# Kernel optimization log

Hardware: AMD Instinct MI355X
Metric: run time of the kernel (lower is better)

Reference implementation:

```python
import jax, jax.numpy as jnp
import numpy as np

B, T = 64, 2048
HID, FAST, SLOW, VOCAB = 256, 64, 256, 64
WRITE_THRESH = 0.4
NEG = -1000000000.0


def setup_inputs() -> dict:
    key = jax.random.key(0)
    ks = jax.random.split(key, 10)
    s = 0.05  # small init so gate sigmoids are not saturated
    return {
        "seq": jax.random.randint(ks[0], (B, T), 0, VOCAB),
        "emb": jax.random.normal(ks[1], (VOCAB, HID), jnp.float32),        # encoder embedding table
        "Wg": jax.random.normal(ks[2], (HID, 1), jnp.float32) * s,         # write_gate
        "bg": jnp.zeros((1,), jnp.float32),
        "Wd": jax.random.normal(ks[3], (HID, 1), jnp.float32) * s,         # demotion_net
        "bd": jnp.zeros((1,), jnp.float32),
        "Wq": jax.random.normal(ks[4], (HID, HID), jnp.float32) * s,       # read_head.q_proj
        "bq": jnp.zeros((HID,), jnp.float32),
        "Wo": jax.random.normal(ks[5], (HID, VOCAB), jnp.float32) * s,     # read_head.out
        "bo": jnp.zeros((VOCAB,), jnp.float32),
    }


def _process_sequence(h, Wg, bg, Wd, bd):
    # h: (B, T, H). Sequential LRU tiered-memory scatter, vectorized over batch.
    Bb, Tt, H = h.shape

    def step(state, tok_h):
        fm, sm, fa, sa, fu, su = state
        ws = jax.nn.sigmoid(tok_h @ Wg + bg)[:, 0]          # (B,) write score
        act = ws >= WRITE_THRESH                            # skip rows with score < 0.4
        fa = fa + fu.astype(jnp.int32)                      # age occupied slots
        sa = sa + su.astype(jnp.int32)
        free = ~fu
        has_free = jnp.any(free, axis=1)                    # (B,)
        free_idx = jnp.argmax(free, axis=1)                 # first free fast slot
        dem = ((fm @ Wd)[..., 0] + bd[0])                   # (B, FAST) demotion scores
        dem_slot = jnp.argmin(dem, axis=1)
        fslot = jnp.where(has_free, free_idx, dem_slot)     # fast slot to write
        foh = jax.nn.one_hot(fslot, FAST, dtype=bool)
        wf = act[:, None] & foh                              # (B, FAST) fast-write mask
        # value demoted to slow (only used when fast was full)
        demoted = jnp.take_along_axis(fm, fslot[:, None, None], axis=1)[:, 0, :]
        slow_act = act & ~has_free
        sfree = ~su
        s_has_free = jnp.any(sfree, axis=1)
        ss = jnp.where(s_has_free, jnp.argmax(sfree, axis=1), jnp.argmax(sa, axis=1))
        soh = jax.nn.one_hot(ss, SLOW, dtype=bool)
        wsm = slow_act[:, None] & soh                        # (B, SLOW) slow-write mask
        sm = jnp.where(wsm[..., None], demoted[:, None, :], sm)
        sa = jnp.where(wsm, 0, sa)
        su = su | wsm
        tok = jax.lax.stop_gradient(tok_h)                   # original writes tok_h.detach()
        fm = jnp.where(wf[..., None], tok[:, None, :], fm)
        fa = jnp.where(wf, 0, fa)
        fu = fu | wf
        return (fm, sm, fa, sa, fu, su), None

    init = (
        jnp.zeros((Bb, FAST, H), h.dtype),
        jnp.zeros((Bb, SLOW, H), h.dtype),
        jnp.zeros((Bb, FAST), jnp.int32),
        jnp.zeros((Bb, SLOW), jnp.int32),
        jnp.zeros((Bb, FAST), bool),
        jnp.zeros((Bb, SLOW), bool),
    )
    hs = jnp.swapaxes(h[:, : Tt - 3], 0, 1)                  # loop runs for T-3 tokens
    (fm, sm, fa, sa, fu, su), _ = jax.lax.scan(step, init, hs)
    memory = jnp.concatenate([fm, sm], axis=1)               # (B, F+S, H)
    mask = jnp.concatenate([fu, su], axis=1).astype(h.dtype)
    slow_mask = su.astype(h.dtype)
    return memory, mask, slow_mask


def reference(seq, emb, Wg, bg, Wd, bd, Wq, bq, Wo, bo):
    h = emb[seq]                                             # encoder: (B, T, H)
    memory, mask, slow_mask = _process_sequence(h, Wg, bg, Wd, bd)
    # ReadHead
    q = h[:, -1, :] @ Wq + bq                                # (B, H)
    scores = jnp.einsum("bnh,bh->bn", memory, q)
    scores = jnp.where(mask == 0, NEG, scores)
    attn = jax.nn.softmax(scores, axis=-1)
    ctx = jnp.einsum("bn,bnh->bh", attn, memory)
    logits = ctx @ Wo + bo                                   # (B, VOCAB)
    return logits, slow_mask
```

## Files before the change

kernel.cpp:

```cpp
#include <hip/hip_runtime.h>
#include <math.h>

#define BB 64
#define TT 2048
#define HIDD 256
#define FASTN 64
#define SLOWN 256
#define VOC 64
#define TLOOP (TT - 3)
#define NEGC -1000000000.0f
#define EPAD 257
#define NEGBIG (-(1 << 20))
#define BYTEAT(U, J) ((int)(((U) >> (8 * (J))) & 0xFFu))

__global__ __launch_bounds__(256) void k_tab(
    const float* __restrict__ emb,
    const float* __restrict__ Wg, const float* __restrict__ bg,
    const float* __restrict__ Wd, const float* __restrict__ bd,
    const float* __restrict__ Wq, const float* __restrict__ bq,
    float* __restrict__ qTok, int* __restrict__ prG, int* __restrict__ invG) {
  const int tid = threadIdx.x;
  __shared__ float eS[HIDD];
  __shared__ float part[4][64];
  __shared__ float demS[64];

  if (blockIdx.x < 256) {
    const int u = blockIdx.x >> 2, jt = blockIdx.x & 3;
    eS[tid] = emb[u * HIDD + tid];
    __syncthreads();
    const int j = tid & 63, kp = tid >> 6;
    const float* w = &Wq[(kp * 64) * HIDD + jt * 64 + j];
    const float* e = &eS[kp * 64];
    float acc = 0.f;
#pragma unroll 8
    for (int kk = 0; kk < 64; ++kk) acc += e[kk] * w[kk * HIDD];
    part[kp][j] = acc;
    __syncthreads();
    if (tid < 64)
      qTok[u * HIDD + jt * 64 + tid] =
          part[0][tid] + part[1][tid] + part[2][tid] + part[3][tid] + bq[jt * 64 + tid];
  } else {
    const int v = tid & 63, kp = tid >> 6;
    const float* e = &emb[v * HIDD + kp * 64];
    const float* wg = &Wg[kp * 64];
    const float* wd = &Wd[kp * 64];
    float g = 0.f, d = 0.f;
#pragma unroll 8
    for (int k = 0; k < 64; ++k) { float ev = e[k]; g += ev * wg[k]; d += ev * wd[k]; }
    part[kp][v] = g;
    __syncthreads();
    __shared__ float dpart[4][64];
    dpart[kp][v] = d;
    __syncthreads();
    int myact = 0;
    if (tid < 64) {
      float gg = part[0][tid] + part[1][tid] + part[2][tid] + part[3][tid] + bg[0];
      float dd = dpart[0][tid] + dpart[1][tid] + dpart[2][tid] + dpart[3][tid] + bd[0];
      myact = (1.f / (1.f + expf(-gg)) >= 0.4f) ? 1 : 0;
      demS[tid] = dd;
    }
    __syncthreads();
    if (tid < 64) {
      float dv = demS[tid];
      int r = 0;
      for (int u2 = 0; u2 < 64; ++u2) {
        float du = demS[u2];
        r += (du < dv || (du == dv && u2 < tid)) ? 1 : 0;
      }
      prG[tid] = myact ? r : 0xFF;
      invG[r] = tid;
    }
  }
}

__global__ __launch_bounds__(512) void k_main(
    const int* __restrict__ seq, const float* __restrict__ emb,
    const float* __restrict__ qTok, const int* __restrict__ prG,
    const int* __restrict__ invG,
    const float* __restrict__ Wo, const float* __restrict__ bo,
    float* __restrict__ out) {
  const int b = blockIdx.x;
  const int tid = threadIdx.x;
  const int lane = tid & 63;
  const int wv = tid >> 6;

  __shared__ float embS[VOC * EPAD];
  __shared__ float WoS[HIDD * VOC];
  __shared__ __align__(16) unsigned char zsB[2080];
  __shared__ float qLastS[HIDD], ctxS[HIDD];
  __shared__ float pp[4][64];
  __shared__ float wS[64];
  __shared__ int prS[64], invS[64], cntTok[64];
  __shared__ int CS[8];
  __shared__ int PsS[8][64], QsS[8][64], aEndS[8][64], eSS[8][64];

  const int4 sq = ((const int4*)(seq + b * TT))[tid];
  const int lastv = seq[b * TT + TT - 1];
  if (tid < 64) { prS[tid] = prG[tid]; invS[tid] = invG[tid]; }
  if (tid < 256) qLastS[tid] = qTok[lastv * HIDD + tid];
  const float4* emb4 = (const float4*)emb;
  for (int i = tid; i < VOC * 64; i += 512) {
    float4 e = emb4[i];
    float* d = &embS[(i >> 6) * EPAD + ((i & 63) << 2)];
    d[0] = e.x; d[1] = e.y; d[2] = e.z; d[3] = e.w;
  }
  {
    const float4* Wo4 = (const float4*)Wo;
    float4* WoS4 = (float4*)WoS;
    for (int i = tid; i < HIDD * VOC / 4; i += 512) WoS4[i] = Wo4[i];
  }
  __syncthreads();

  const int t0 = tid * 4;
  int tk[4] = {sq.x, sq.y, sq.z, sq.w};
  int by[4]; int c = 0;
#pragma unroll
  for (int j = 0; j < 4; ++j) {
    int r = prS[tk[j]];
    by[j] = (t0 + j < TLOOP) ? r : 0xFF;
    c += (by[j] != 0xFF) ? 1 : 0;
  }
  int incl = c;
  for (int s = 1; s < 64; s <<= 1) {
    int t = __shfl_up(incl, s);
    if (lane >= s) incl += t;
  }
  if (lane == 63) CS[wv] = incl;
  __syncthreads();

  int Ow = 0, A = 0;
#pragma unroll
  for (int w2 = 0; w2 < 8; ++w2) {
    int cw = CS[w2];
    Ow += (w2 < wv) ? cw : 0;
    A += cw;
  }
  {
    int pos = Ow + incl - c;
#pragma unroll
    for (int j = 0; j < 4; ++j)
      if (by[j] != 0xFF) zsB[pos++] = (unsigned char)by[j];
  }
  __syncthreads();

  const int fsplit = A < 64 ? A : 64;
  const int nL = A - fsplit;
  const int win = nL < 256 ? nL : 256;
  const int wstart = A - win;
  const int L = (((A + 7) >> 3) + 15) & ~15;
  const int baseW = wv * L;
  const int endW = min(baseW + L, A);

  int P = 0, Q = NEGBIG;
  for (int g = baseW; g < endW; g += 16) {
    uint4 t4 = *(const uint4*)(zsB + g);
    unsigned dsw[4] = {t4.x, t4.y, t4.z, t4.w};
    const int gHi = min(g + 16, endW);
    if (gHi == g + 16 && gHi <= fsplit) {
#pragma unroll
      for (int d = 0; d < 4; ++d)
#pragma unroll
        for (int j = 0; j < 4; ++j) {
          int x = (BYTEAT(dsw[d], j) <= lane) ? 1 : 0;
          P += x; Q += x;
        }
    } else if (gHi == g + 16 && g >= fsplit) {
#pragma unroll
      for (int d = 0; d < 4; ++d)
#pragma unroll
        for (int j = 0; j < 4; ++j) {
          int x = (BYTEAT(dsw[d], j) <= lane) ? 1 : 0;
          P += x - 1;
          Q = max(Q + x - 1, x);
        }
    } else {
#pragma unroll
      for (int d = 0; d < 4; ++d)
#pragma unroll
        for (int j = 0; j < 4; ++j) {
          int i = g + d * 4 + j;
          int x = (BYTEAT(dsw[d], j) <= lane) ? 1 : 0;
          bool vld = i < endW;
          bool fil = i < fsplit;
          int p = fil ? x : x - 1;
          int q = fil ? NEGBIG : x;
          int Pn = P + p;
          int Qn = max(Q + p, q);
          P = vld ? Pn : P;
          Q = vld ? Qn : Q;
        }
    }
  }
  PsS[wv][lane] = P;
  QsS[wv][lane] = Q;
  __syncthreads();

  int a = 0;
  for (int w2 = 0; w2 < wv; ++w2)
    a = max(a + PsS[w2][lane], QsS[w2][lane]);

  int e = 0;
  for (int g = baseW; g < endW; g += 16) {
    uint4 t4 = *(const uint4*)(zsB + g);
    unsigned dsw[4] = {t4.x, t4.y, t4.z, t4.w};
    const int gHi = min(g + 16, endW);
    const bool full = (gHi == g + 16);
    if (full && gHi <= fsplit) {
#pragma unroll
      for (int d = 0; d < 4; ++d)
#pragma unroll
        for (int j = 0; j < 4; ++j)
          a += (BYTEAT(dsw[d], j) <= lane) ? 1 : 0;
    } else if (full && g >= fsplit && gHi <= wstart) {
#pragma unroll
      for (int d = 0; d < 4; ++d)
#pragma unroll
        for (int j = 0; j < 4; ++j) {
          int xm1 = (BYTEAT(dsw[d], j) <= lane) ? 0 : -1;
          a = max(a, 1) + xm1;
        }
    } else if (full && g >= wstart) {
#pragma unroll
      for (int d = 0; d < 4; ++d)
#pragma unroll
        for (int j = 0; j < 4; ++j) {
          int xm1 = (BYTEAT(dsw[d], j) <= lane) ? 0 : -1;
          e += (a > 0) ? 1 : 0;
          a = max(a, 1) + xm1;
        }
    } else {
#pragma unroll
      for (int d = 0; d < 4; ++d)
#pragma unroll
        for (int j = 0; j < 4; ++j) {
          int i = g + d * 4 + j;
          int x = (BYTEAT(dsw[d], j) <= lane) ? 1 : 0;
          bool vld = i < endW;
          bool fil = i < fsplit;
          bool wg = vld && (i >= wstart);
          e += (wg && a > 0) ? 1 : 0;
          int af = a + x;
          int al = max(a, 1) + (x - 1);
          int an = fil ? af : al;
          a = vld ? an : a;
        }
    }
  }
  aEndS[wv][lane] = a;
  eSS[wv][lane] = e;
  __syncthreads();

  if (tid < 64) {
    int af = aEndS[7][lane];
    int et = 0;
#pragma unroll
    for (int w2 = 0; w2 < 8; ++w2) et += eSS[w2][lane];
    int ap = __shfl_up(af, 1); if (lane == 0) ap = 0;
    int ep = __shfl_up(et, 1); if (lane == 0) ep = 0;
    cntTok[invS[lane]] = (af - ap) + (et - ep);
  }
  __syncthreads();

  if (tid < 256) {
    int v = tid & 63, part = tid >> 6;
    const float* er = &embS[v * EPAD + part * 64];
    const float* qr = &qLastS[part * 64];
    float s = 0.f;
#pragma unroll 8
    for (int k = 0; k < 64; ++k) s += er[k] * qr[k];
    pp[part][v] = s;
  }
  __syncthreads();
  if (tid < 64) {
    float sc = pp[0][tid] + pp[1][tid] + pp[2][tid] + pp[3][tid];
    int cc = cntTok[tid];
    float m = (cc > 0) ? sc : NEGC;
    for (int off = 32; off; off >>= 1) m = fmaxf(m, __shfl_xor(m, off));
    float w = (cc > 0) ? (float)cc * expf(sc - m) : 0.f;
    float z = w;
    for (int off = 32; off; off >>= 1) z += __shfl_xor(z, off);
    z += (float)(FASTN + SLOWN - (fsplit + win)) * expf(NEGC - m);
    wS[tid] = w / z;
  }
  __syncthreads();

  if (tid < 256) {
    float cacc = 0.f;
#pragma unroll 8
    for (int u = 0; u < 64; ++u) cacc += wS[u] * embS[u * EPAD + tid];
    ctxS[tid] = cacc;
  }
  __syncthreads();

  if (tid < 256) {
    int o = tid & 63, part = tid >> 6;
    const float* cr = &ctxS[part * 64];
    const float* wr = &WoS[part * 64 * VOC + o];
    float s = 0.f;
#pragma unroll 8
    for (int k = 0; k < 64; ++k) s += cr[k] * wr[k * VOC];
    pp[part][o] = s;
  }
  __syncthreads();
  if (tid < 64)
    out[b * VOC + tid] = pp[0][tid] + pp[1][tid] + pp[2][tid] + pp[3][tid] + bo[tid];
  if (tid < 256)
    out[BB * VOC + b * SLOWN + tid] = (tid < win) ? 1.0f : 0.0f;
}

extern "C" void kernel_launch(void* const* d_in, const int* in_sizes, int n_in,
                              void* d_out, int out_size, void* d_ws, size_t ws_size,
                              hipStream_t stream) {
  const int*   seq = (const int*)d_in[0];
  const float* emb = (const float*)d_in[1];
  const float* Wg  = (const float*)d_in[2];
  const float* bg  = (const float*)d_in[3];
  const float* Wd  = (const float*)d_in[4];
  const float* bd  = (const float*)d_in[5];
  const float* Wq  = (const float*)d_in[6];
  const float* bq  = (const float*)d_in[7];
  const float* Wo  = (const float*)d_in[8];
  const float* bo  = (const float*)d_in[9];
  float* out = (float*)d_out;

  char* ws = (char*)d_ws;
  float* qTok = (float*)ws;
  int*   prG  = (int*)(ws + 16384 * 4);
  int*   invG = (int*)(ws + 16448 * 4);

  k_tab<<<dim3(257), dim3(256), 0, stream>>>(emb, Wg, bg, Wd, bd, Wq, bq,
                                             qTok, prG, invG);
  k_main<<<dim3(64), dim3(512), 0, stream>>>(seq, emb, qTok, prG, invG,
                                             Wo, bo, out);
}
```

Measured before the change: 94.90 us.

## Fuse table precompute kernel into main kernel, computing per-block in shared memory

Removes the separate k_tab launch. Each block of the main kernel now computes the gate/demotion scores and rank tables from shared-memory embeddings, and only the query projection for its last token. This drops one kernel launch and the global workspace round trip, and avoids projecting all 64 vocab rows through Wq. The cost is redundant gate/rank computation in every block and a serial Wq read per block.

```diff
diff --git a/kernel.cpp b/kernel.cpp
--- a/kernel.cpp
+++ b/kernel.cpp
@@ -13,70 +13,11 @@
 #define NEGBIG (-(1 << 20))
 #define BYTEAT(U, J) ((int)(((U) >> (8 * (J))) & 0xFFu))
 
-__global__ __launch_bounds__(256) void k_tab(
-    const float* __restrict__ emb,
+__global__ __launch_bounds__(512) void k_one(
+    const int* __restrict__ seq, const float* __restrict__ emb,
     const float* __restrict__ Wg, const float* __restrict__ bg,
     const float* __restrict__ Wd, const float* __restrict__ bd,
     const float* __restrict__ Wq, const float* __restrict__ bq,
-    float* __restrict__ qTok, int* __restrict__ prG, int* __restrict__ invG) {
-  const int tid = threadIdx.x;
-  __shared__ float eS[HIDD];
-  __shared__ float part[4][64];
-  __shared__ float demS[64];
-
-  if (blockIdx.x < 256) {
-    const int u = blockIdx.x >> 2, jt = blockIdx.x & 3;
-    eS[tid] = emb[u * HIDD + tid];
-    __syncthreads();
-    const int j = tid & 63, kp = tid >> 6;
-    const float* w = &Wq[(kp * 64) * HIDD + jt * 64 + j];
-    const float* e = &eS[kp * 64];
-    float acc = 0.f;
-#pragma unroll 8
-    for (int kk = 0; kk < 64; ++kk) acc += e[kk] * w[kk * HIDD];
-    part[kp][j] = acc;
-    __syncthreads();
-    if (tid < 64)
-      qTok[u * HIDD + jt * 64 + tid] =
-          part[0][tid] + part[1][tid] + part[2][tid] + part[3][tid] + bq[jt * 64 + tid];
-  } else {
-    const int v = tid & 63, kp = tid >> 6;
-    const float* e = &emb[v * HIDD + kp * 64];
-    const float* wg = &Wg[kp * 64];
-    const float* wd = &Wd[kp * 64];
-    float g = 0.f, d = 0.f;
-#pragma unroll 8
-    for (int k = 0; k < 64; ++k) { float ev = e[k]; g += ev * wg[k]; d += ev * wd[k]; }
-    part[kp][v] = g;
-    __syncthreads();
-    __shared__ float dpart[4][64];
-    dpart[kp][v] = d;
-    __syncthreads();
-    int myact = 0;
-    if (tid < 64) {
-      float gg = part[0][tid] + part[1][tid] + part[2][tid] + part[3][tid] + bg[0];
-      float dd = dpart[0][tid] + dpart[1][tid] + dpart[2][tid] + dpart[3][tid] + bd[0];
-      myact = (1.f / (1.f + expf(-gg)) >= 0.4f) ? 1 : 0;
-      demS[tid] = dd;
-    }
-    __syncthreads();
-    if (tid < 64) {
-      float dv = demS[tid];
-      int r = 0;
-      for (int u2 = 0; u2 < 64; ++u2) {
-        float du = demS[u2];
-        r += (du < dv || (du == dv && u2 < tid)) ? 1 : 0;
-      }
-      prG[tid] = myact ? r : 0xFF;
-      invG[r] = tid;
-    }
-  }
-}
-
-__global__ __launch_bounds__(512) void k_main(
-    const int* __restrict__ seq, const float* __restrict__ emb,
-    const float* __restrict__ qTok, const int* __restrict__ prG,
-    const int* __restrict__ invG,
     const float* __restrict__ Wo, const float* __restrict__ bo,
     float* __restrict__ out) {
   const int b = blockIdx.x;
@@ -89,15 +30,15 @@
   __shared__ __align__(16) unsigned char zsB[2080];
   __shared__ float qLastS[HIDD], ctxS[HIDD];
   __shared__ float pp[4][64];
-  __shared__ float wS[64];
+  __shared__ float gp8[8][64], dp8[8][64];
+  __shared__ float qp2[2][HIDD];
+  __shared__ float demS[64], wS[64];
   __shared__ int prS[64], invS[64], cntTok[64];
   __shared__ int CS[8];
   __shared__ int PsS[8][64], QsS[8][64], aEndS[8][64], eSS[8][64];
 
   const int4 sq = ((const int4*)(seq + b * TT))[tid];
   const int lastv = seq[b * TT + TT - 1];
-  if (tid < 64) { prS[tid] = prG[tid]; invS[tid] = invG[tid]; }
-  if (tid < 256) qLastS[tid] = qTok[lastv * HIDD + tid];
   const float4* emb4 = (const float4*)emb;
   for (int i = tid; i < VOC * 64; i += 512) {
     float4 e = emb4[i];
@@ -108,6 +49,38 @@
     const float4* Wo4 = (const float4*)Wo;
     float4* WoS4 = (float4*)WoS;
     for (int i = tid; i < HIDD * VOC / 4; i += 512) WoS4[i] = Wo4[i];
+  }
+  __syncthreads();
+
+  {
+    const int v = tid & 63, kp = tid >> 6;
+    const float* er = &embS[v * EPAD + kp * 32];
+    const float* wg = &Wg[kp * 32];
+    const float* wd = &Wd[kp * 32];
+    float g = 0.f, d = 0.f;
+#pragma unroll 8
+    for (int k = 0; k < 32; ++k) { float e = er[k]; g += e * wg[k]; d += e * wd[k]; }
+    gp8[kp][v] = g; dp8[kp][v] = d;
+  }
+  __syncthreads();
+  if (tid < 64) {
+    float g = bg[0], d = bd[0];
+#pragma unroll
+    for (int p = 0; p < 8; ++p) { g += gp8[p][tid]; d += dp8[p][tid]; }
+    int act = (1.f / (1.f + expf(-g)) >= 0.4f) ? 1 : 0;
+    demS[tid] = d;
+    prS[tid] = act;
+  }
+  __syncthreads();
+  if (tid < 64) {
+    float dv = demS[tid];
+    int r = 0;
+    for (int u2 = 0; u2 < 64; ++u2) {
+      float du = demS[u2];
+      r += (du < dv || (du == dv && u2 < tid)) ? 1 : 0;
+    }
+    invS[r] = tid;
+    prS[tid] = prS[tid] ? r : 0xFF;
   }
   __syncthreads();
 
@@ -259,6 +232,18 @@
     int ep = __shfl_up(et, 1); if (lane == 0) ep = 0;
     cntTok[invS[lane]] = (af - ap) + (et - ep);
   }
+
+  {
+    const int j = tid & 255, half = tid >> 8;
+    const float* eL = &embS[lastv * EPAD + half * 128];
+    const float* wq = &Wq[(half * 128) * HIDD + j];
+    float acc = 0.f;
+#pragma unroll 8
+    for (int k = 0; k < 128; ++k) acc += eL[k] * wq[k * HIDD];
+    qp2[half][j] = acc;
+  }
+  __syncthreads();
+  if (tid < 256) qLastS[tid] = qp2[0][tid] + qp2[1][tid] + bq[tid];
   __syncthreads();
 
   if (tid < 256) {
@@ -323,13 +308,6 @@
   const float* bo  = (const float*)d_in[9];
   float* out = (float*)d_out;
 
-  char* ws = (char*)d_ws;
-  float* qTok = (float*)ws;
-  int*   prG  = (int*)(ws + 16384 * 4);
-  int*   invG = (int*)(ws + 16448 * 4);
-
-  k_tab<<<dim3(257), dim3(256), 0, stream>>>(emb, Wg, bg, Wd, bd, Wq, bq,
-                                             qTok, prG, invG);
-  k_main<<<dim3(64), dim3(512), 0, stream>>>(seq, emb, qTok, prG, invG,
-                                             Wo, bo, out);
+  k_one<<<dim3(64), dim3(512), 0, stream>>>(seq, emb, Wg, bg, Wd, bd,
+                                            Wq, bq, Wo, bo, out);
 }
```

Result: no change. 94.71 us (-0.2%).
